# Performance work log

Hardware: AMD Instinct MI355X
Metric: run time of the kernel (lower is better)

The kernel has to match this reference:

```python
import jax, jax.numpy as jnp
import numpy as np
from jax import lax

BATCH = 8192
HID = 10
IN = 64
STEPS = 512
REVERSE = True


def setup_inputs() -> dict:
    key = jax.random.key(0)
    ks = jax.random.split(key, 9)
    s_in = 1.0 / np.sqrt(HID)
    return {
        "hidden": jax.random.normal(ks[0], (1, BATCH, HID), dtype=jnp.float32),
        "w_ih": jax.random.uniform(ks[1], (3 * HID, IN), jnp.float32, -s_in, s_in),
        "w_hh": jax.random.uniform(ks[2], (3 * HID, HID), jnp.float32, -s_in, s_in),
        "b_ih": jax.random.uniform(ks[3], (3 * HID,), jnp.float32, -s_in, s_in),
        "b_hh": jax.random.uniform(ks[4], (3 * HID,), jnp.float32, -s_in, s_in),
        "l1_w": jax.random.uniform(ks[5], (10, HID), jnp.float32, -s_in, s_in),
        "l1_b": jax.random.uniform(ks[6], (10,), jnp.float32, -s_in, s_in),
        "l2_w": jax.random.uniform(ks[7], (IN, 10), jnp.float32, -s_in, s_in),
        "l2_b": jax.random.uniform(ks[8], (IN,), jnp.float32, -s_in, s_in),
        "step": STEPS,
    }


def _gru_cell(h, x, w_ih, w_hh, b_ih, b_hh):
    # PyTorch GRU gate order: reset, update, new
    gi = x @ w_ih.T + b_ih  # [B, 3H]
    gh = h @ w_hh.T + b_hh  # [B, 3H]
    i_r, i_z, i_n = jnp.split(gi, 3, axis=-1)
    h_r, h_z, h_n = jnp.split(gh, 3, axis=-1)
    r = jax.nn.sigmoid(i_r + h_r)
    z = jax.nn.sigmoid(i_z + h_z)
    n = jnp.tanh(i_n + r * h_n)
    return (1.0 - z) * n + z * h


def reference(hidden, w_ih, w_hh, b_ih, b_hh, l1_w, l1_b, l2_w, l2_b, step):
    h0 = hidden[0]  # [B, H]
    B = h0.shape[0]
    x0 = jnp.zeros((B, IN), dtype=h0.dtype)  # first GRU input is zeros

    def body(carry, _):
        h, x = carry
        h_new = _gru_cell(h, x, w_ih, w_hh, b_ih, b_hh)
        o = h_new @ l1_w.T + l1_b          # l1 on GRU output
        x_next = o @ l2_w.T + l2_b         # l2 feeds next GRU step
        return (h_new, x_next), o

    _, outs = lax.scan(body, (h0, x0), None, length=step)  # [T, B, 10]
    outs = jnp.transpose(outs, (1, 0, 2))  # [B, T, 10]
    if REVERSE:
        outs = outs[:, ::-1, :]
    return outs
```

## Files before the change

kernel.cpp:

```cpp
#include <hip/hip_runtime.h>

#define HID 10
#define STEPS 512

typedef __attribute__((ext_vector_type(2))) float v2f;
typedef __attribute__((ext_vector_type(4))) float v4f;

template<int F>
static __device__ __forceinline__ float swz(float v) {
    return __int_as_float(__builtin_amdgcn_ds_swizzle(__float_as_int(v), (F << 5) | 0x10));
}

__attribute__((amdgpu_waves_per_eu(2, 2)))
__global__ __launch_bounds__(64) void gru_decoder_kernel(
    const float* __restrict__ hidden, const float* __restrict__ w_ih,
    const float* __restrict__ w_hh, const float* __restrict__ b_ih,
    const float* __restrict__ b_hh, const float* __restrict__ l1_w,
    const float* __restrict__ l1_b, const float* __restrict__ l2_w,
    const float* __restrict__ l2_b, float* __restrict__ out)
{
    __shared__ float sWx[640];
    __shared__ float sbx[64];
    __shared__ float sWgi[300];
    __shared__ float sbgi[30];
    __shared__ float sWhh[300];
    __shared__ float sH[64];

    const int lane = threadIdx.x;
    const int f    = lane & 15;
    const int g    = lane >> 4;
    const int b    = blockIdx.x * 4 + g;
    const bool ok  = (f < HID);
    const int fi   = ok ? f : 0;

    for (int e = lane; e < 640; e += 64) {
        int i = e / 10, j = e - i * 10;
        float acc = 0.f;
        #pragma unroll
        for (int k = 0; k < 10; ++k) acc += l2_w[i * 10 + k] * l1_w[k * 10 + j];
        sWx[e] = acc;
    }
    {
        float acc = l2_b[lane];
        #pragma unroll
        for (int k = 0; k < 10; ++k) acc += l2_w[lane * 10 + k] * l1_b[k];
        sbx[lane] = acc;
    }
    for (int e = lane; e < 300; e += 64) sWhh[e] = w_hh[e];
    __syncthreads();
    for (int e = lane; e < 300; e += 64) {
        int m = e / 10, j = e - m * 10;
        float acc = 0.f;
        for (int k = 0; k < 64; ++k) acc += w_ih[m * 64 + k] * sWx[k * 10 + j];
        sWgi[e] = acc;
    }
    if (lane < 30) {
        float acc = b_ih[lane];
        for (int k = 0; k < 64; ++k) acc += w_ih[lane * 64 + k] * sbx[k];
        sbgi[lane] = acc;
    }
    __syncthreads();

    const float LOG2E = 1.4426950408889634f;
    const float S2    = 2.f * LOG2E;

    #define MKW(k2)                                                              \
        const int k0_##k2 = 2 * (k2), k1_##k2 = 2 * (k2) + 1;                    \
        const v2f wr##k2 = ok ? v2f{                                             \
            -(sWgi[fi * 10 + k0_##k2] + sWhh[fi * 10 + k0_##k2]) * LOG2E,        \
            -(sWgi[fi * 10 + k1_##k2] + sWhh[fi * 10 + k1_##k2]) * LOG2E}        \
            : v2f{0.f, 0.f};                                                     \
        const v2f wz##k2 = ok ? v2f{                                             \
            -(sWgi[(10 + fi) * 10 + k0_##k2] + sWhh[(10 + fi) * 10 + k0_##k2]) * LOG2E, \
            -(sWgi[(10 + fi) * 10 + k1_##k2] + sWhh[(10 + fi) * 10 + k1_##k2]) * LOG2E} \
            : v2f{0.f, 0.f};                                                     \
        const v2f wi##k2 = ok ? v2f{                                             \
            sWgi[(20 + fi) * 10 + k0_##k2] * S2,                                 \
            sWgi[(20 + fi) * 10 + k1_##k2] * S2} : v2f{0.f, 0.f};                \
        const v2f wh##k2 = ok ? v2f{                                             \
            sWhh[(20 + fi) * 10 + k0_##k2] * S2,                                 \
            sWhh[(20 + fi) * 10 + k1_##k2] * S2} : v2f{0.f, 0.f};                \
        const v2f wo##k2 = ok ? v2f{                                             \
            l1_w[fi * 10 + k0_##k2], l1_w[fi * 10 + k1_##k2]} : v2f{0.f, 0.f};
    MKW(0) MKW(1) MKW(2) MKW(3) MKW(4)
    #undef MKW

    const float br = ok ? -(sbgi[fi] + b_hh[fi]) * LOG2E : 0.f;
    const float bz = ok ? -(sbgi[10 + fi] + b_hh[10 + fi]) * LOG2E : 0.f;
    const float bi = ok ? sbgi[20 + fi] * S2 : 0.f;
    const float bh = ok ? b_hh[20 + fi] * S2 : 0.f;
    const float bo = ok ? l1_b[fi] : 0.f;
    const v2f BR2 = {br, 0.f}, BZ2 = {bz, 0.f}, BI2 = {bi, 0.f},
              BH2 = {bh, 0.f}, BO2 = {bo, 0.f};
    const float br0_ = ok ? -(b_ih[fi] + b_hh[fi]) * LOG2E : 0.f;
    const float bz0_ = ok ? -(b_ih[10 + fi] + b_hh[10 + fi]) * LOG2E : 0.f;
    const float bni0 = ok ? b_ih[20 + fi] * S2 : 0.f;

    float h = ok ? hidden[(size_t)b * HID + f] : 0.f;

    float* pb = out + (size_t)b * (STEPS * HID) + (size_t)(STEPS - 1) * HID + f;
    float* sHrow = &sH[g * 16];

    {
        float ha[10];
        ha[0] = swz<0>(h); ha[1] = swz<1>(h); ha[2] = swz<2>(h);
        ha[3] = swz<3>(h); ha[4] = swz<4>(h); ha[5] = swz<5>(h);
        ha[6] = swz<6>(h); ha[7] = swz<7>(h); ha[8] = swz<8>(h);
        ha[9] = swz<9>(h);
        float pr = 0.f, pz = 0.f, ph = 0.f;
        #pragma unroll
        for (int k = 0; k < 10; ++k) {
            pr += sWhh[fi * 10 + k] * ha[k];
            pz += sWhh[(10 + fi) * 10 + k] * ha[k];
            ph += sWhh[(20 + fi) * 10 + k] * ha[k];
        }
        float vr = br0_ - pr * LOG2E;
        float vz = bz0_ - pz * LOG2E;
        float r = __builtin_amdgcn_rcpf(1.f + __builtin_amdgcn_exp2f(vr));
        float z = __builtin_amdgcn_rcpf(1.f + __builtin_amdgcn_exp2f(vz));
        float y = bni0 + r * (ph * S2 + bh);
        float n = 1.f - 2.f * __builtin_amdgcn_rcpf(1.f + __builtin_amdgcn_exp2f(y));
        h = ok ? (n + z * (h - n)) : 0.f;
    }

    #pragma unroll 1
    for (int t = 1; t < STEPS; ++t) {
        sHrow[f] = h;
        __builtin_amdgcn_wave_barrier();
        __builtin_amdgcn_sched_barrier(0);
        v4f q0 = *(const v4f*)(sHrow);
        v4f q1 = *(const v4f*)(sHrow + 4);
        v2f q2 = *(const v2f*)(sHrow + 8);

        v2f h2_0 = __builtin_shufflevector(q0, q0, 0, 1);
        v2f h2_1 = __builtin_shufflevector(q0, q0, 2, 3);
        v2f h2_2 = __builtin_shufflevector(q1, q1, 0, 1);
        v2f h2_3 = __builtin_shufflevector(q1, q1, 2, 3);
        v2f h2_4 = q2;

        v2f ar = wr0 * h2_0 + BR2;
        v2f az = wz0 * h2_0 + BZ2;
        v2f ai = wi0 * h2_0 + BI2;
        v2f ah = wh0 * h2_0 + BH2;
        v2f ao = wo0 * h2_0 + BO2;
        ar += wr1 * h2_1; az += wz1 * h2_1; ai += wi1 * h2_1;
        ah += wh1 * h2_1; ao += wo1 * h2_1;
        ar += wr2 * h2_2; az += wz2 * h2_2; ai += wi2 * h2_2;
        ah += wh2 * h2_2; ao += wo2 * h2_2;
        ar += wr3 * h2_3; az += wz3 * h2_3; ai += wi3 * h2_3;
        ah += wh3 * h2_3; ao += wo3 * h2_3;
        ar += wr4 * h2_4; az += wz4 * h2_4; ai += wi4 * h2_4;
        ah += wh4 * h2_4; ao += wo4 * h2_4;

        float arx = ar.x + ar.y;
        float azx = az.x + az.y;
        float aix = ai.x + ai.y;
        float ahx = ah.x + ah.y;
        float o   = ao.x + ao.y;

        float er = __builtin_amdgcn_exp2f(arx);
        float r  = __builtin_amdgcn_rcpf(1.f + er);
        float ez = __builtin_amdgcn_exp2f(azx);
        float y  = __builtin_fmaf(r, ahx, aix);
        float en = __builtin_amdgcn_exp2f(y);
        float p  = en * ez;
        float tt = h - ez;
        float u  = p + tt;
        float num = __builtin_fmaf(h, en, u);
        float v   = en + ez;
        float den = (p + v) + 1.f;
        h = num * __builtin_amdgcn_rcpf(den);

        if (ok) pb[0] = o;
        pb -= HID;
    }

    {
        v2f h2_0 = {swz<0>(h), swz<1>(h)};
        v2f h2_1 = {swz<2>(h), swz<3>(h)};
        v2f h2_2 = {swz<4>(h), swz<5>(h)};
        v2f h2_3 = {swz<6>(h), swz<7>(h)};
        v2f h2_4 = {swz<8>(h), swz<9>(h)};
        v2f ao = wo0 * h2_0 + BO2;
        ao += wo1 * h2_1;
        ao += wo2 * h2_2;
        ao += wo3 * h2_3;
        ao += wo4 * h2_4;
        if (ok) pb[0] = ao.x + ao.y;
    }
}

extern "C" void kernel_launch(void* const* d_in, const int* in_sizes, int n_in,
                              void* d_out, int out_size, void* d_ws, size_t ws_size,
                              hipStream_t stream) {
    (void)in_sizes; (void)n_in; (void)d_ws; (void)ws_size; (void)out_size;
    dim3 grid(2048), block(64);
    gru_decoder_kernel<<<grid, block, 0, stream>>>(
        (const float*)d_in[0], (const float*)d_in[1], (const float*)d_in[2],
        (const float*)d_in[3], (const float*)d_in[4], (const float*)d_in[5],
        (const float*)d_in[6], (const float*)d_in[7], (const float*)d_in[8],
        (float*)d_out);
}
```

Before: 292.2 us.

## Interleave two independent batch groups per wave to hide recurrence latency

Each wave now processes eight batch rows as two independent groups, A and B, and alternates their GRU steps so one chain's LDS round trip and transcendental latency can overlap with the other's arithmetic. The grid is halved and waves_per_eu drops from 2 to 1, giving the kernel more registers. The LDS reload of h now sits right after each store, and the explicit wave_barrier and sched_barrier are removed from the loop. This trades hardware wave-level parallelism for instruction-level parallelism within a wave, and relies on LDS ordering within a single wave holding without those barriers.

```diff
diff --git a/kernel.cpp b/kernel.cpp
--- a/kernel.cpp
+++ b/kernel.cpp
@@ -11,7 +11,7 @@
     return __int_as_float(__builtin_amdgcn_ds_swizzle(__float_as_int(v), (F << 5) | 0x10));
 }
 
-__attribute__((amdgpu_waves_per_eu(2, 2)))
+__attribute__((amdgpu_waves_per_eu(1, 1)))
 __global__ __launch_bounds__(64) void gru_decoder_kernel(
     const float* __restrict__ hidden, const float* __restrict__ w_ih,
     const float* __restrict__ w_hh, const float* __restrict__ b_ih,
@@ -24,12 +24,13 @@
     __shared__ float sWgi[300];
     __shared__ float sbgi[30];
     __shared__ float sWhh[300];
-    __shared__ float sH[64];
+    __shared__ float sH[128];
 
     const int lane = threadIdx.x;
     const int f    = lane & 15;
     const int g    = lane >> 4;
-    const int b    = blockIdx.x * 4 + g;
+    const int bA   = blockIdx.x * 8 + g;
+    const int bB   = bA + 4;
     const bool ok  = (f < HID);
     const int fi   = ok ? f : 0;
 
@@ -96,12 +97,15 @@
     const float bz0_ = ok ? -(b_ih[10 + fi] + b_hh[10 + fi]) * LOG2E : 0.f;
     const float bni0 = ok ? b_ih[20 + fi] * S2 : 0.f;
 
-    float h = ok ? hidden[(size_t)b * HID + f] : 0.f;
-
-    float* pb = out + (size_t)b * (STEPS * HID) + (size_t)(STEPS - 1) * HID + f;
-    float* sHrow = &sH[g * 16];
-
-    {
+    float hA = ok ? hidden[(size_t)bA * HID + f] : 0.f;
+    float hB = ok ? hidden[(size_t)bB * HID + f] : 0.f;
+
+    float* pbA = out + (size_t)bA * (STEPS * HID) + (size_t)(STEPS - 1) * HID + f;
+    float* pbB = out + (size_t)bB * (STEPS * HID) + (size_t)(STEPS - 1) * HID + f;
+    float* rowA = &sH[g * 16];
+    float* rowB = &sH[(4 + g) * 16];
+
+    auto peel0 = [&](float& h) {
         float ha[10];
         ha[0] = swz<0>(h); ha[1] = swz<1>(h); ha[2] = swz<2>(h);
         ha[3] = swz<3>(h); ha[4] = swz<4>(h); ha[5] = swz<5>(h);
@@ -121,23 +125,24 @@
         float y = bni0 + r * (ph * S2 + bh);
         float n = 1.f - 2.f * __builtin_amdgcn_rcpf(1.f + __builtin_amdgcn_exp2f(y));
         h = ok ? (n + z * (h - n)) : 0.f;
-    }
-
-    #pragma unroll 1
-    for (int t = 1; t < STEPS; ++t) {
-        sHrow[f] = h;
-        __builtin_amdgcn_wave_barrier();
-        __builtin_amdgcn_sched_barrier(0);
-        v4f q0 = *(const v4f*)(sHrow);
-        v4f q1 = *(const v4f*)(sHrow + 4);
-        v2f q2 = *(const v2f*)(sHrow + 8);
-
+    };
+    peel0(hA);
+    peel0(hB);
+
+    rowA[f] = hA;
+    rowB[f] = hB;
+    __builtin_amdgcn_wave_barrier();
+    v4f qA0 = *(const v4f*)(rowA); v4f qA1 = *(const v4f*)(rowA + 4);
+    v2f qA2 = *(const v2f*)(rowA + 8);
+    v4f qB0 = *(const v4f*)(rowB); v4f qB1 = *(const v4f*)(rowB + 4);
+    v2f qB2 = *(const v2f*)(rowB + 8);
+
+    auto gru_step = [&](v4f q0, v4f q1, v2f q2, float& h, float& o) {
         v2f h2_0 = __builtin_shufflevector(q0, q0, 0, 1);
         v2f h2_1 = __builtin_shufflevector(q0, q0, 2, 3);
         v2f h2_2 = __builtin_shufflevector(q1, q1, 0, 1);
         v2f h2_3 = __builtin_shufflevector(q1, q1, 2, 3);
         v2f h2_4 = q2;
-
         v2f ar = wr0 * h2_0 + BR2;
         v2f az = wz0 * h2_0 + BZ2;
         v2f ai = wi0 * h2_0 + BI2;
@@ -151,13 +156,11 @@
         ah += wh3 * h2_3; ao += wo3 * h2_3;
         ar += wr4 * h2_4; az += wz4 * h2_4; ai += wi4 * h2_4;
         ah += wh4 * h2_4; ao += wo4 * h2_4;
-
         float arx = ar.x + ar.y;
         float azx = az.x + az.y;
         float aix = ai.x + ai.y;
         float ahx = ah.x + ah.y;
-        float o   = ao.x + ao.y;
-
+        o = ao.x + ao.y;
         float er = __builtin_amdgcn_exp2f(arx);
         float r  = __builtin_amdgcn_rcpf(1.f + er);
         float ez = __builtin_amdgcn_exp2f(azx);
@@ -170,23 +173,39 @@
         float v   = en + ez;
         float den = (p + v) + 1.f;
         h = num * __builtin_amdgcn_rcpf(den);
-
-        if (ok) pb[0] = o;
-        pb -= HID;
+    };
+
+    #pragma unroll 1
+    for (int t = 1; t < STEPS; ++t) {
+        float oA, oB;
+        gru_step(qA0, qA1, qA2, hA, oA);
+        rowA[f] = hA;
+        qA0 = *(const v4f*)(rowA);
+        qA1 = *(const v4f*)(rowA + 4);
+        qA2 = *(const v2f*)(rowA + 8);
+        if (ok) pbA[0] = oA;
+        pbA -= HID;
+        gru_step(qB0, qB1, qB2, hB, oB);
+        rowB[f] = hB;
+        qB0 = *(const v4f*)(rowB);
+        qB1 = *(const v4f*)(rowB + 4);
+        qB2 = *(const v2f*)(rowB + 8);
+        if (ok) pbB[0] = oB;
+        pbB -= HID;
     }
 
     {
-        v2f h2_0 = {swz<0>(h), swz<1>(h)};
-        v2f h2_1 = {swz<2>(h), swz<3>(h)};
-        v2f h2_2 = {swz<4>(h), swz<5>(h)};
-        v2f h2_3 = {swz<6>(h), swz<7>(h)};
-        v2f h2_4 = {swz<8>(h), swz<9>(h)};
-        v2f ao = wo0 * h2_0 + BO2;
-        ao += wo1 * h2_1;
-        ao += wo2 * h2_2;
-        ao += wo3 * h2_3;
-        ao += wo4 * h2_4;
-        if (ok) pb[0] = ao.x + ao.y;
+        v2f aoA = wo0 * __builtin_shufflevector(qA0, qA0, 0, 1) + BO2;
+        aoA += wo1 * __builtin_shufflevector(qA0, qA0, 2, 3);
+        aoA += wo2 * __builtin_shufflevector(qA1, qA1, 0, 1);
+        aoA += wo3 * __builtin_shufflevector(qA1, qA1, 2, 3);
+        aoA += wo4 * qA2;
+        v2f aoB = wo0 * __builtin_shufflevector(qB0, qB0, 0, 1) + BO2;
+        aoB += wo1 * __builtin_shufflevector(qB0, qB0, 2, 3);
+        aoB += wo2 * __builtin_shufflevector(qB1, qB1, 0, 1);
+        aoB += wo3 * __builtin_shufflevector(qB1, qB1, 2, 3);
+        aoB += wo4 * qB2;
+        if (ok) { pbA[0] = aoA.x + aoA.y; pbB[0] = aoB.x + aoB.y; }
     }
 }
 
@@ -194,7 +213,7 @@
                               void* d_out, int out_size, void* d_ws, size_t ws_size,
                               hipStream_t stream) {
     (void)in_sizes; (void)n_in; (void)d_ws; (void)ws_size; (void)out_size;
-    dim3 grid(2048), block(64);
+    dim3 grid(1024), block(64);
     gru_decoder_kernel<<<grid, block, 0, stream>>>(
         (const float*)d_in[0], (const float*)d_in[1], (const float*)d_in[2],
         (const float*)d_in[3], (const float*)d_in[4], (const float*)d_in[5],
```

New measurement: 332.5 us. 1.14x slower.
